# Optimization experiments

Measured on AMD Instinct MI355X. Metric: run time of the kernel, lower is better.

## Reference

```python
import jax, jax.numpy as jnp
import numpy as np

B, C, T, S = 128, 64, 8192, 16

def setup_inputs() -> dict:
    key = jax.random.key(0)
    k1, k2, k3, k4 = jax.random.split(key, 4)
    x = jax.random.normal(k1, (B, C, T), dtype=jnp.float32)
    subj_idx = jax.random.randint(k2, (B,), 0, S)
    # per-subject 1x1 conv == per-subject [C, C] matrix + bias.
    # (original identity-inits; we use identity + small noise so the op is non-trivial)
    W = jnp.eye(C, dtype=jnp.float32)[None] + 0.02 * jax.random.normal(k3, (S, C, C), dtype=jnp.float32)
    b = 0.02 * jax.random.normal(k4, (S, C), dtype=jnp.float32)
    return {"x": x, "subj_idx": subj_idx, "W": W, "b": b}

def reference(x, subj_idx, W, b):
    # Hard routing: gather each sample's subject weight, then batched 1x1 conv.
    Wb = W[subj_idx]            # [B, C_out, C_in]
    bb = b[subj_idx]            # [B, C_out]
    # out[b, o, t] = sum_c Wb[b, o, c] * x[b, c, t] + bb[b, o]
    return jnp.einsum('boc,bct->bot', Wb, x) + bb[:, :, None]
```

## Files before the change

### kernel.cpp

```cpp
#include <hip/hip_runtime.h>
#include <hip/hip_bf16.h>


typedef __attribute__((ext_vector_type(8))) short  bf16x8;
typedef __attribute__((ext_vector_type(16))) float f32x16;

namespace {
constexpr int Cdim  = 64;
constexpr int Tdim  = 8192;
constexpr int TT    = 256;
constexpr int STR   = TT + 4;
constexpr int BLOCK = 256;
}

static __device__ __forceinline__ short f2bf(float f) {
    return (short)__builtin_bit_cast(unsigned short, __float2bfloat16(f));
}

__global__ __launch_bounds__(BLOCK, 2)
void subject_layers_r6(const float* __restrict__ x,
                       const int*   __restrict__ subj,
                       const float* __restrict__ W,
                       const float* __restrict__ bias,
                       float*       __restrict__ out) {
    __shared__ float tile[Cdim * STR];

    const int b    = blockIdx.y;
    const int tb   = blockIdx.x;
    const int tid  = threadIdx.x;
    const int wave = tid >> 6;
    const int lane = tid & 63;
    const int hi   = lane >> 5;
    const int ln   = lane & 31;
    const int s    = subj[b];

    const size_t xbase = (size_t)b * Cdim * Tdim + (size_t)tb * TT;

    {
        float4 v[4];
        #pragma unroll
        for (int gg = 0; gg < 4; ++gg) {
            #pragma unroll
            for (int g = 0; g < 4; ++g) {
                const int row = (gg * 4 + g) * 4 + wave;
                v[g] = *reinterpret_cast<const float4*>(x + xbase + (size_t)row * Tdim + lane * 4);
            }
            #pragma unroll
            for (int g = 0; g < 4; ++g) {
                const int row = (gg * 4 + g) * 4 + wave;
                *reinterpret_cast<float4*>(&tile[row * STR + lane * 4]) = v[g];
            }
        }
    }

    bf16x8 afrag[2][4];
    const float* Wb = W + (size_t)s * Cdim * Cdim;
    #pragma unroll
    for (int ot = 0; ot < 2; ++ot) {
        #pragma unroll
        for (int kb = 0; kb < 4; ++kb) {
            const float* ap = Wb + (size_t)(ot * 32 + ln) * Cdim + kb * 16 + hi * 8;
            const float4 a0 = *reinterpret_cast<const float4*>(ap);
            const float4 a1 = *reinterpret_cast<const float4*>(ap + 4);
            bf16x8 f;
            f[0] = f2bf(a0.x); f[1] = f2bf(a0.y); f[2] = f2bf(a0.z); f[3] = f2bf(a0.w);
            f[4] = f2bf(a1.x); f[5] = f2bf(a1.y); f[6] = f2bf(a1.z); f[7] = f2bf(a1.w);
            afrag[ot][kb] = f;
        }
    }

    f32x16 bini[2];
    const float* bb = bias + (size_t)s * Cdim;
    #pragma unroll
    for (int ot = 0; ot < 2; ++ot)
        #pragma unroll
        for (int r = 0; r < 16; ++r)
            bini[ot][r] = bb[ot * 32 + (r & 3) + 8 * (r >> 2) + 4 * hi];

    __syncthreads();

    bf16x8 bfrag[2][4];
    #pragma unroll
    for (int st = 0; st < 2; ++st) {
        const int col = wave * 64 + st * 32 + ln;
        #pragma unroll
        for (int kb = 0; kb < 4; ++kb) {
            bf16x8 f;
            #pragma unroll
            for (int j = 0; j < 8; ++j)
                f[j] = f2bf(tile[(kb * 16 + hi * 8 + j) * STR + col]);
            bfrag[st][kb] = f;
        }
    }

    __syncthreads();

    #pragma unroll
    for (int st = 0; st < 2; ++st) {
        const int col = wave * 64 + st * 32 + ln;
        #pragma unroll
        for (int ot = 0; ot < 2; ++ot) {
            f32x16 acc = bini[ot];
            #pragma unroll
            for (int kb = 0; kb < 4; ++kb)
                acc = __builtin_amdgcn_mfma_f32_32x32x16_bf16(afrag[ot][kb], bfrag[st][kb], acc, 0, 0, 0);
            #pragma unroll
            for (int r = 0; r < 16; ++r)
                tile[(ot * 32 + (r & 3) + 8 * (r >> 2) + 4 * hi) * STR + col] = acc[r];
        }
    }

    __syncthreads();

    #pragma unroll
    for (int g = 0; g < 16; ++g) {
        const int row = g * 4 + wave;
        const float4 v = *reinterpret_cast<const float4*>(&tile[row * STR + lane * 4]);
        *reinterpret_cast<float4*>(out + xbase + (size_t)row * Tdim + lane * 4) = v;
    }
}

extern "C" void kernel_launch(void* const* d_in, const int* in_sizes, int n_in,
                              void* d_out, int out_size, void* d_ws, size_t ws_size,
                              hipStream_t stream) {
    const float* x    = (const float*)d_in[0];
    const int*   subj = (const int*)  d_in[1];
    const float* W    = (const float*)d_in[2];
    const float* bias = (const float*)d_in[3];
    float*       out  = (float*)d_out;

    const int B = in_sizes[1];
    dim3 grid(Tdim / TT, B);
    dim3 block(BLOCK);
    hipLaunchKernelGGL(subject_layers_r6, grid, block, 0, stream,
                       x, subj, W, bias, out);
}
```

Baseline: 105.3 us.

## Make blocks persistent over eight time tiles with register prefetch of next tile

Each block now processes eight consecutive 256-column time tiles instead of one, loading W fragments and bias once and reusing them across tiles. The next tile's x data is prefetched into registers while the current tile is converted, multiplied and stored, which overlaps global loads with compute. The LDS row padding is removed, so the column-wise bf16 fragment reads and accumulator writes may now hit more bank conflicts. The grid shrinks eightfold to 512 blocks, which lowers parallelism and may leave the GPU less fully occupied on a memory-bound op.

```diff
diff --git a/kernel.cpp b/kernel.cpp
--- a/kernel.cpp
+++ b/kernel.cpp
@@ -9,7 +9,7 @@
 constexpr int Cdim  = 64;
 constexpr int Tdim  = 8192;
 constexpr int TT    = 256;
-constexpr int STR   = TT + 4;
+constexpr int TILES = 8;
 constexpr int BLOCK = 256;
 }
 
@@ -18,15 +18,15 @@
 }
 
 __global__ __launch_bounds__(BLOCK, 2)
-void subject_layers_r6(const float* __restrict__ x,
+void subject_layers_r8(const float* __restrict__ x,
                        const int*   __restrict__ subj,
                        const float* __restrict__ W,
                        const float* __restrict__ bias,
                        float*       __restrict__ out) {
-    __shared__ float tile[Cdim * STR];
+    __shared__ float tile[Cdim * TT];
 
     const int b    = blockIdx.y;
-    const int tb   = blockIdx.x;
+    const int tg   = blockIdx.x;
     const int tid  = threadIdx.x;
     const int wave = tid >> 6;
     const int lane = tid & 63;
@@ -34,24 +34,8 @@
     const int ln   = lane & 31;
     const int s    = subj[b];
 
-    const size_t xbase = (size_t)b * Cdim * Tdim + (size_t)tb * TT;
-
-    {
-        float4 v[4];
-        #pragma unroll
-        for (int gg = 0; gg < 4; ++gg) {
-            #pragma unroll
-            for (int g = 0; g < 4; ++g) {
-                const int row = (gg * 4 + g) * 4 + wave;
-                v[g] = *reinterpret_cast<const float4*>(x + xbase + (size_t)row * Tdim + lane * 4);
-            }
-            #pragma unroll
-            for (int g = 0; g < 4; ++g) {
-                const int row = (gg * 4 + g) * 4 + wave;
-                *reinterpret_cast<float4*>(&tile[row * STR + lane * 4]) = v[g];
-            }
-        }
-    }
+    const size_t bbase  = (size_t)b * Cdim * Tdim;
+    const size_t tstart = (size_t)tg * (TILES * TT);
 
     bf16x8 afrag[2][4];
     const float* Wb = W + (size_t)s * Cdim * Cdim;
@@ -77,46 +61,79 @@
         for (int r = 0; r < 16; ++r)
             bini[ot][r] = bb[ot * 32 + (r & 3) + 8 * (r >> 2) + 4 * hi];
 
-    __syncthreads();
-
-    bf16x8 bfrag[2][4];
-    #pragma unroll
-    for (int st = 0; st < 2; ++st) {
-        const int col = wave * 64 + st * 32 + ln;
-        #pragma unroll
-        for (int kb = 0; kb < 4; ++kb) {
-            bf16x8 f;
-            #pragma unroll
-            for (int j = 0; j < 8; ++j)
-                f[j] = f2bf(tile[(kb * 16 + hi * 8 + j) * STR + col]);
-            bfrag[st][kb] = f;
-        }
-    }
-
-    __syncthreads();
-
-    #pragma unroll
-    for (int st = 0; st < 2; ++st) {
-        const int col = wave * 64 + st * 32 + ln;
-        #pragma unroll
-        for (int ot = 0; ot < 2; ++ot) {
-            f32x16 acc = bini[ot];
-            #pragma unroll
-            for (int kb = 0; kb < 4; ++kb)
-                acc = __builtin_amdgcn_mfma_f32_32x32x16_bf16(afrag[ot][kb], bfrag[st][kb], acc, 0, 0, 0);
-            #pragma unroll
-            for (int r = 0; r < 16; ++r)
-                tile[(ot * 32 + (r & 3) + 8 * (r >> 2) + 4 * hi) * STR + col] = acc[r];
-        }
-    }
-
-    __syncthreads();
-
+    float4 v[16];
     #pragma unroll
     for (int g = 0; g < 16; ++g) {
         const int row = g * 4 + wave;
-        const float4 v = *reinterpret_cast<const float4*>(&tile[row * STR + lane * 4]);
-        *reinterpret_cast<float4*>(out + xbase + (size_t)row * Tdim + lane * 4) = v;
+        v[g] = *reinterpret_cast<const float4*>(
+            x + bbase + tstart + (size_t)row * Tdim + lane * 4);
+    }
+    #pragma unroll
+    for (int g = 0; g < 16; ++g) {
+        const int row = g * 4 + wave;
+        *reinterpret_cast<float4*>(&tile[row * TT + lane * 4]) = v[g];
+    }
+    __syncthreads();
+
+    for (int k = 0; k < TILES; ++k) {
+        const size_t toff = tstart + (size_t)k * TT;
+
+        if (k + 1 < TILES) {
+            #pragma unroll
+            for (int g = 0; g < 16; ++g) {
+                const int row = g * 4 + wave;
+                v[g] = *reinterpret_cast<const float4*>(
+                    x + bbase + toff + TT + (size_t)row * Tdim + lane * 4);
+            }
+        }
+
+        bf16x8 bfrag[2][4];
+        #pragma unroll
+        for (int st = 0; st < 2; ++st) {
+            const int col = wave * 64 + st * 32 + ln;
+            #pragma unroll
+            for (int kb = 0; kb < 4; ++kb) {
+                bf16x8 f;
+                #pragma unroll
+                for (int j = 0; j < 8; ++j)
+                    f[j] = f2bf(tile[(kb * 16 + hi * 8 + j) * TT + col]);
+                bfrag[st][kb] = f;
+            }
+        }
+        __syncthreads();
+
+        #pragma unroll
+        for (int st = 0; st < 2; ++st) {
+            const int col = wave * 64 + st * 32 + ln;
+            #pragma unroll
+            for (int ot = 0; ot < 2; ++ot) {
+                f32x16 acc = bini[ot];
+                #pragma unroll
+                for (int kb = 0; kb < 4; ++kb)
+                    acc = __builtin_amdgcn_mfma_f32_32x32x16_bf16(
+                        afrag[ot][kb], bfrag[st][kb], acc, 0, 0, 0);
+                #pragma unroll
+                for (int r = 0; r < 16; ++r)
+                    tile[(ot * 32 + (r & 3) + 8 * (r >> 2) + 4 * hi) * TT + col] = acc[r];
+            }
+        }
+        __syncthreads();
+
+        #pragma unroll
+        for (int g = 0; g < 16; ++g) {
+            const int row = g * 4 + wave;
+            const float4 o4 = *reinterpret_cast<const float4*>(&tile[row * TT + lane * 4]);
+            *reinterpret_cast<float4*>(
+                out + bbase + toff + (size_t)row * Tdim + lane * 4) = o4;
+        }
+        if (k + 1 < TILES) {
+            #pragma unroll
+            for (int g = 0; g < 16; ++g) {
+                const int row = g * 4 + wave;
+                *reinterpret_cast<float4*>(&tile[row * TT + lane * 4]) = v[g];
+            }
+        }
+        __syncthreads();
     }
 }
 
@@ -130,8 +147,8 @@
     float*       out  = (float*)d_out;
 
     const int B = in_sizes[1];
-    dim3 grid(Tdim / TT, B);
+    dim3 grid(Tdim / (TILES * TT), B);
     dim3 block(BLOCK);
-    hipLaunchKernelGGL(subject_layers_r6, grid, block, 0, stream,
+    hipLaunchKernelGGL(subject_layers_r8, grid, block, 0, stream,
                        x, subj, W, bias, out);
 }
```

New measurement: 235.8 us. 2.24x slower.

## Store LDS tile as bf16, raise occupancy, fuse fragment load with MFMA

Applied to the files above, without the earlier changes.

The shared-memory staging tile now holds bf16 values instead of fp32, which roughly halves LDS usage. Launch bounds rise from 2 to 4 blocks per CU, and the barrier between building fragments and running the MFMAs is removed by processing each sub-tile in place within its own wave. The cost of under-occupancy and of the extra sync is the target. The trade-off is that outputs are now rounded to bf16 before being widened back to fp32, which adds a second quantization step. The unpadded tile may also introduce LDS bank conflicts on the column reads.

```diff
diff --git a/kernel.cpp b/kernel.cpp
--- a/kernel.cpp
+++ b/kernel.cpp
@@ -9,21 +9,24 @@
 constexpr int Cdim  = 64;
 constexpr int Tdim  = 8192;
 constexpr int TT    = 256;
-constexpr int STR   = TT + 4;
 constexpr int BLOCK = 256;
 }
 
-static __device__ __forceinline__ short f2bf(float f) {
-    return (short)__builtin_bit_cast(unsigned short, __float2bfloat16(f));
+static __device__ __forceinline__ unsigned short f2bfu(float f) {
+    return __builtin_bit_cast(unsigned short, __float2bfloat16(f));
+}
+static __device__ __forceinline__ float bf2f(unsigned short u) {
+    const unsigned int v = ((unsigned int)u) << 16;
+    return __builtin_bit_cast(float, v);
 }
 
-__global__ __launch_bounds__(BLOCK, 2)
-void subject_layers_r6(const float* __restrict__ x,
+__global__ __launch_bounds__(BLOCK, 4)
+void subject_layers_r9(const float* __restrict__ x,
                        const int*   __restrict__ subj,
                        const float* __restrict__ W,
                        const float* __restrict__ bias,
                        float*       __restrict__ out) {
-    __shared__ float tile[Cdim * STR];
+    __shared__ unsigned short tile[Cdim * TT];
 
     const int b    = blockIdx.y;
     const int tb   = blockIdx.x;
@@ -43,12 +46,16 @@
             #pragma unroll
             for (int g = 0; g < 4; ++g) {
                 const int row = (gg * 4 + g) * 4 + wave;
-                v[g] = *reinterpret_cast<const float4*>(x + xbase + (size_t)row * Tdim + lane * 4);
+                v[g] = *reinterpret_cast<const float4*>(
+                    x + xbase + (size_t)row * Tdim + lane * 4);
             }
             #pragma unroll
             for (int g = 0; g < 4; ++g) {
                 const int row = (gg * 4 + g) * 4 + wave;
-                *reinterpret_cast<float4*>(&tile[row * STR + lane * 4]) = v[g];
+                ushort4 u;
+                u.x = f2bfu(v[g].x); u.y = f2bfu(v[g].y);
+                u.z = f2bfu(v[g].z); u.w = f2bfu(v[g].w);
+                *reinterpret_cast<ushort4*>(&tile[row * TT + lane * 4]) = u;
             }
         }
     }
@@ -63,8 +70,10 @@
             const float4 a0 = *reinterpret_cast<const float4*>(ap);
             const float4 a1 = *reinterpret_cast<const float4*>(ap + 4);
             bf16x8 f;
-            f[0] = f2bf(a0.x); f[1] = f2bf(a0.y); f[2] = f2bf(a0.z); f[3] = f2bf(a0.w);
-            f[4] = f2bf(a1.x); f[5] = f2bf(a1.y); f[6] = f2bf(a1.z); f[7] = f2bf(a1.w);
+            f[0] = (short)f2bfu(a0.x); f[1] = (short)f2bfu(a0.y);
+            f[2] = (short)f2bfu(a0.z); f[3] = (short)f2bfu(a0.w);
+            f[4] = (short)f2bfu(a1.x); f[5] = (short)f2bfu(a1.y);
+            f[6] = (short)f2bfu(a1.z); f[7] = (short)f2bfu(a1.w);
             afrag[ot][kb] = f;
         }
     }
@@ -79,34 +88,31 @@
 
     __syncthreads();
 
-    bf16x8 bfrag[2][4];
     #pragma unroll
     for (int st = 0; st < 2; ++st) {
         const int col = wave * 64 + st * 32 + ln;
+
+        bf16x8 bfrag[4];
         #pragma unroll
         for (int kb = 0; kb < 4; ++kb) {
             bf16x8 f;
             #pragma unroll
             for (int j = 0; j < 8; ++j)
-                f[j] = f2bf(tile[(kb * 16 + hi * 8 + j) * STR + col]);
-            bfrag[st][kb] = f;
+                f[j] = (short)tile[(kb * 16 + hi * 8 + j) * TT + col];
+            bfrag[kb] = f;
         }
-    }
 
-    __syncthreads();
-
-    #pragma unroll
-    for (int st = 0; st < 2; ++st) {
-        const int col = wave * 64 + st * 32 + ln;
         #pragma unroll
         for (int ot = 0; ot < 2; ++ot) {
             f32x16 acc = bini[ot];
             #pragma unroll
             for (int kb = 0; kb < 4; ++kb)
-                acc = __builtin_amdgcn_mfma_f32_32x32x16_bf16(afrag[ot][kb], bfrag[st][kb], acc, 0, 0, 0);
+                acc = __builtin_amdgcn_mfma_f32_32x32x16_bf16(
+                    afrag[ot][kb], bfrag[kb], acc, 0, 0, 0);
             #pragma unroll
             for (int r = 0; r < 16; ++r)
-                tile[(ot * 32 + (r & 3) + 8 * (r >> 2) + 4 * hi) * STR + col] = acc[r];
+                tile[(ot * 32 + (r & 3) + 8 * (r >> 2) + 4 * hi) * TT + col] =
+                    f2bfu(acc[r]);
         }
     }
 
@@ -115,8 +121,10 @@
     #pragma unroll
     for (int g = 0; g < 16; ++g) {
         const int row = g * 4 + wave;
-        const float4 v = *reinterpret_cast<const float4*>(&tile[row * STR + lane * 4]);
-        *reinterpret_cast<float4*>(out + xbase + (size_t)row * Tdim + lane * 4) = v;
+        const ushort4 u = *reinterpret_cast<const ushort4*>(&tile[row * TT + lane * 4]);
+        float4 o4;
+        o4.x = bf2f(u.x); o4.y = bf2f(u.y); o4.z = bf2f(u.z); o4.w = bf2f(u.w);
+        *reinterpret_cast<float4*>(out + xbase + (size_t)row * Tdim + lane * 4) = o4;
     }
 }
 
@@ -132,6 +140,6 @@
     const int B = in_sizes[1];
     dim3 grid(Tdim / TT, B);
     dim3 block(BLOCK);
-    hipLaunchKernelGGL(subject_layers_r6, grid, block, 0, stream,
+    hipLaunchKernelGGL(subject_layers_r9, grid, block, 0, stream,
                        x, subj, W, bias, out);
 }
```

Result: no change. 104.9 us (-0.4%).

## Load input directly into LDS and store MFMA results straight to global

Applied to the files above, without the earlier changes.

Input rows are copied into shared memory with global_load_lds, which skips register staging and the row padding. MFMA accumulators are written directly to global memory, so the LDS write-back of outputs and two barriers are gone. Each output store becomes a scalar access of 32 contiguous floats per row instead of a float4 copy out of LDS. That may cut store coalescing efficiency in a kernel that is already bandwidth-bound.

```diff
diff --git a/kernel.cpp b/kernel.cpp
--- a/kernel.cpp
+++ b/kernel.cpp
@@ -9,7 +9,6 @@
 constexpr int Cdim  = 64;
 constexpr int Tdim  = 8192;
 constexpr int TT    = 256;
-constexpr int STR   = TT + 4;
 constexpr int BLOCK = 256;
 }
 
@@ -18,12 +17,12 @@
 }
 
 __global__ __launch_bounds__(BLOCK, 2)
-void subject_layers_r6(const float* __restrict__ x,
-                       const int*   __restrict__ subj,
-                       const float* __restrict__ W,
-                       const float* __restrict__ bias,
-                       float*       __restrict__ out) {
-    __shared__ float tile[Cdim * STR];
+void subject_layers_r10(const float* __restrict__ x,
+                        const int*   __restrict__ subj,
+                        const float* __restrict__ W,
+                        const float* __restrict__ bias,
+                        float*       __restrict__ out) {
+    __shared__ float tile[Cdim * TT];
 
     const int b    = blockIdx.y;
     const int tb   = blockIdx.x;
@@ -36,21 +35,15 @@
 
     const size_t xbase = (size_t)b * Cdim * Tdim + (size_t)tb * TT;
 
-    {
-        float4 v[4];
-        #pragma unroll
-        for (int gg = 0; gg < 4; ++gg) {
-            #pragma unroll
-            for (int g = 0; g < 4; ++g) {
-                const int row = (gg * 4 + g) * 4 + wave;
-                v[g] = *reinterpret_cast<const float4*>(x + xbase + (size_t)row * Tdim + lane * 4);
-            }
-            #pragma unroll
-            for (int g = 0; g < 4; ++g) {
-                const int row = (gg * 4 + g) * 4 + wave;
-                *reinterpret_cast<float4*>(&tile[row * STR + lane * 4]) = v[g];
-            }
-        }
+    #pragma unroll
+    for (int g = 0; g < 16; ++g) {
+        const int row = g * 4 + wave;
+        __builtin_amdgcn_global_load_lds(
+            (const __attribute__((address_space(1))) unsigned int*)
+                (x + xbase + (size_t)row * Tdim + lane * 4),
+            (__attribute__((address_space(3))) unsigned int*)
+                (&tile[row * TT]),
+            16, 0, 0);
     }
 
     bf16x8 afrag[2][4];
@@ -79,44 +72,33 @@
 
     __syncthreads();
 
-    bf16x8 bfrag[2][4];
+    float* ob = out + xbase;
     #pragma unroll
     for (int st = 0; st < 2; ++st) {
         const int col = wave * 64 + st * 32 + ln;
+
+        bf16x8 bfrag[4];
         #pragma unroll
         for (int kb = 0; kb < 4; ++kb) {
             bf16x8 f;
             #pragma unroll
             for (int j = 0; j < 8; ++j)
-                f[j] = f2bf(tile[(kb * 16 + hi * 8 + j) * STR + col]);
-            bfrag[st][kb] = f;
+                f[j] = f2bf(tile[(kb * 16 + hi * 8 + j) * TT + col]);
+            bfrag[kb] = f;
         }
-    }
 
-    __syncthreads();
-
-    #pragma unroll
-    for (int st = 0; st < 2; ++st) {
-        const int col = wave * 64 + st * 32 + ln;
         #pragma unroll
         for (int ot = 0; ot < 2; ++ot) {
             f32x16 acc = bini[ot];
             #pragma unroll
             for (int kb = 0; kb < 4; ++kb)
-                acc = __builtin_amdgcn_mfma_f32_32x32x16_bf16(afrag[ot][kb], bfrag[st][kb], acc, 0, 0, 0);
+                acc = __builtin_amdgcn_mfma_f32_32x32x16_bf16(
+                    afrag[ot][kb], bfrag[kb], acc, 0, 0, 0);
             #pragma unroll
             for (int r = 0; r < 16; ++r)
-                tile[(ot * 32 + (r & 3) + 8 * (r >> 2) + 4 * hi) * STR + col] = acc[r];
+                ob[(size_t)(ot * 32 + (r & 3) + 8 * (r >> 2) + 4 * hi) * Tdim + col]
+                    = acc[r];
         }
-    }
-
-    __syncthreads();
-
-    #pragma unroll
-    for (int g = 0; g < 16; ++g) {
-        const int row = g * 4 + wave;
-        const float4 v = *reinterpret_cast<const float4*>(&tile[row * STR + lane * 4]);
-        *reinterpret_cast<float4*>(out + xbase + (size_t)row * Tdim + lane * 4) = v;
     }
 }
 
@@ -132,6 +114,6 @@
     const int B = in_sizes[1];
     dim3 grid(Tdim / TT, B);
     dim3 block(BLOCK);
-    hipLaunchKernelGGL(subject_layers_r6, grid, block, 0, stream,
+    hipLaunchKernelGGL(subject_layers_r10, grid, block, 0, stream,
                        x, subj, W, bias, out);
 }
```

New measurement: 104.5 us. About the same (-0.8%).
